# Optimization experiments

Measured on AMD Instinct MI355X. Metric: run time of the kernel, lower is better.

The kernel has to match this reference:

```python
import jax, jax.numpy as jnp
import numpy as np


def setup_inputs() -> dict:
    key = jax.random.key(0)
    k1, k2 = jax.random.split(key)
    T, K, D = 100000, 512, 64
    flags_matrix = jax.random.uniform(k1, (T, K), dtype=jnp.float32)  # ~half > 0.5
    emb_weight = jax.random.normal(k2, (K, D), dtype=jnp.float32)
    return {"flags_matrix": flags_matrix, "emb_weight": emb_weight}


def reference(flags_matrix, emb_weight):
    # mask[t,k] = 1 if flag active; bag-of-embeddings mean over active items per row.
    mask = (flags_matrix > 0.5).astype(emb_weight.dtype)          # [T, K]
    counts = jnp.sum(mask, axis=1, keepdims=True)                  # [T, 1]
    sums = mask @ emb_weight                                       # [T, D] masked sum of embeddings
    # rows with no active flags -> zeros (matches the torch branch)
    return jnp.where(counts > 0, sums / jnp.maximum(counts, 1.0), 0.0)
```

## Files before the change

kernel.cpp:

```cpp
#include <hip/hip_runtime.h>
#include <stdint.h>


#define T_ROWS 100000
#define K_FLAGS 512
#define D_DIM 64
#define TILES (T_ROWS / 16)

typedef __attribute__((ext_vector_type(4))) float f32x4;
typedef __attribute__((ext_vector_type(8))) short bf16x8;

__device__ __forceinline__ uint32_t f32_to_bf16_rne(float f) {
  union { float f; uint32_t u; } v; v.f = f;
  uint32_t u = v.u;
  return (u + 0x7FFFu + ((u >> 16) & 1u)) >> 16;
}

__global__ __launch_bounds__(1024, 8) void flagbag_kernel(const float* __restrict__ flags,
                                                          const float* __restrict__ W,
                                                          float* __restrict__ out) {
  __shared__ uint4 sB[16 * 4 * 64];
  __shared__ uint32_t sM[16][256];

  const int tid = threadIdx.x;

#pragma unroll
  for (int p = 0; p < 4; ++p) {
    const int E  = tid + p * 1024;
    const int s  = E >> 8;
    const int nt = (E >> 6) & 3;
    const int ln = E & 63;
    const int n  = (ln & 15) + 16 * nt;
    const int kq = ln >> 4;
    const int kb = 128 * kq + 8 * s;
    uint32_t r[4];
#pragma unroll
    for (int j = 0; j < 4; ++j) {
      uint32_t lo = f32_to_bf16_rne(W[(size_t)(kb + 2 * j    ) * D_DIM + n]);
      uint32_t hi = f32_to_bf16_rne(W[(size_t)(kb + 2 * j + 1) * D_DIM + n]);
      r[j] = lo | (hi << 16);
    }
    sB[E] = make_uint4(r[0], r[1], r[2], r[3]);
  }
  __syncthreads();

  const int lane = tid & 63;
  const int wave = tid >> 6;
  const int tile = wave * 512 + (int)blockIdx.x;
  if (tile >= TILES) return;

  const int t0 = tile * 16;

  const float* ft = flags + (size_t)t0 * K_FLAGS + lane * 8;

  uint32_t D0 = 0, D1 = 0, D2 = 0, D3 = 0;
  f32x4 ra[4], rb[4];
#pragma unroll
  for (int r = 0; r < 3; ++r) {
    ra[r] = *reinterpret_cast<const f32x4*>(ft + r * K_FLAGS);
    rb[r] = *reinterpret_cast<const f32x4*>(ft + r * K_FLAGS + 4);
  }
#pragma unroll
  for (int r = 0; r < 16; ++r) {
    if (r + 3 < 16) {
      ra[(r + 3) & 3] = *reinterpret_cast<const f32x4*>(ft + (r + 3) * K_FLAGS);
      rb[(r + 3) & 3] = *reinterpret_cast<const f32x4*>(ft + (r + 3) * K_FLAGS + 4);
    }
    const f32x4 a = ra[r & 3], b = rb[r & 3];
    uint32_t byte = 0;
#pragma unroll
    for (int j = 0; j < 4; ++j) {
      byte |= (a[j] > 0.5f) ? (1u << j)       : 0u;
      byte |= (b[j] > 0.5f) ? (1u << (j + 4)) : 0u;
    }
    const uint32_t sh = byte << ((r & 3) * 8);
    if ((r >> 2) == 0) D0 |= sh;
    else if ((r >> 2) == 1) D1 |= sh;
    else if ((r >> 2) == 2) D2 |= sh;
    else D3 |= sh;
  }

  uint32_t* sMw = sM[wave];
  sMw[0 * 64 + (lane ^ 0)]  = D0;
  sMw[1 * 64 + (lane ^ 4)]  = D1;
  sMw[2 * 64 + (lane ^ 8)]  = D2;
  sMw[3 * 64 + (lane ^ 12)] = D3;

  const int m  = lane & 15;
  const int kq = lane >> 4;
  const int mj = m >> 2, mb = m & 3;
  const uint8_t* sMb = reinterpret_cast<const uint8_t*>(sMw);

  uint32_t mbytes[16];
#pragma unroll
  for (int s = 0; s < 16; ++s)
    mbytes[s] = sMb[(size_t)(mj * 64 + ((16 * kq + s) ^ (4 * mj))) * 4 + mb];

  int cnt = 0;
#pragma unroll
  for (int s = 0; s < 16; ++s) cnt += __popc(mbytes[s]);
  cnt += __shfl_xor(cnt, 16);
  cnt += __shfl_xor(cnt, 32);
  const float inv = (cnt > 0) ? (1.0f / (float)cnt) : 0.0f;

  const uint4* sbl = &sB[lane];
  f32x4 acc[4];
#pragma unroll
  for (int nt = 0; nt < 4; ++nt) acc[nt] = (f32x4){0.f, 0.f, 0.f, 0.f};

  uint4 bc[4], bn[4];
#pragma unroll
  for (int nt = 0; nt < 4; ++nt) bc[nt] = sbl[nt * 64];

#pragma unroll
  for (int s = 0; s < 16; ++s) {
    if (s + 1 < 16) {
#pragma unroll
      for (int nt = 0; nt < 4; ++nt) bn[nt] = sbl[((s + 1) * 4 + nt) * 64];
    }
    const uint32_t byte = mbytes[s];
    bf16x8 af;
#pragma unroll
    for (int e = 0; e < 8; ++e) af[e] = ((byte >> e) & 1u) ? (short)0x3F80 : (short)0;

#pragma unroll
    for (int nt = 0; nt < 4; ++nt)
      acc[nt] = __builtin_amdgcn_mfma_f32_16x16x32_bf16(
          af, *reinterpret_cast<const bf16x8*>(&bc[nt]), acc[nt], 0, 0, 0);

#pragma unroll
    for (int nt = 0; nt < 4; ++nt) bc[nt] = bn[nt];
  }

#pragma unroll
  for (int r = 0; r < 4; ++r) {
    const int row = kq * 4 + r;
    const float invr = __shfl(inv, row);
    float* orow = out + (size_t)(t0 + row) * D_DIM + m;
#pragma unroll
    for (int nt = 0; nt < 4; ++nt)
      orow[16 * nt] = acc[nt][r] * invr;
  }
}

extern "C" void kernel_launch(void* const* d_in, const int* in_sizes, int n_in,
                              void* d_out, int out_size, void* d_ws, size_t ws_size,
                              hipStream_t stream) {
  const float* flags = (const float*)d_in[0];
  const float* W     = (const float*)d_in[1];
  float* out         = (float*)d_out;

  hipLaunchKernelGGL(flagbag_kernel, dim3(512), dim3(1024), 0, stream, flags, W, out);
}
```

Measured before the change: 45.69 us.

## Precompute bf16 B fragments in separate kernel and read from global

Moves the per-block conversion of the embedding weights into MFMA bf16 fragments into a small prep kernel that writes a global buffer. The main kernel drops its shared-memory B staging and __syncthreads, reading fragments directly from global/L2, and folds the mask-byte reads and popcount into the MFMA loop. This removes redundant per-block conversion work and the barrier, at the cost of an extra kernel launch and global-memory fragment loads instead of LDS loads inside the inner loop.

```diff
diff --git a/kernel.cpp b/kernel.cpp
--- a/kernel.cpp
+++ b/kernel.cpp
@@ -10,40 +10,37 @@
 typedef __attribute__((ext_vector_type(4))) float f32x4;
 typedef __attribute__((ext_vector_type(8))) short bf16x8;
 
+__device__ uint32_t g_bfrag[16 * 4 * 64 * 4];
+
 __device__ __forceinline__ uint32_t f32_to_bf16_rne(float f) {
   union { float f; uint32_t u; } v; v.f = f;
   uint32_t u = v.u;
   return (u + 0x7FFFu + ((u >> 16) & 1u)) >> 16;
 }
 
+__global__ void prep_b_kernel(const float* __restrict__ W) {
+  int E = blockIdx.x * blockDim.x + threadIdx.x;
+  if (E >= 16 * 4 * 64) return;
+  int lane = E & 63;
+  int nt   = (E >> 6) & 3;
+  int s    = E >> 8;
+  int n    = (lane & 15) + 16 * nt;
+  int kb   = 128 * (lane >> 4) + 8 * s;
+  uint32_t r[4];
+#pragma unroll
+  for (int j = 0; j < 4; ++j) {
+    uint32_t lo = f32_to_bf16_rne(W[(size_t)(kb + 2 * j    ) * D_DIM + n]);
+    uint32_t hi = f32_to_bf16_rne(W[(size_t)(kb + 2 * j + 1) * D_DIM + n]);
+    r[j] = lo | (hi << 16);
+  }
+  *reinterpret_cast<uint4*>(&g_bfrag[(size_t)E * 4]) = make_uint4(r[0], r[1], r[2], r[3]);
+}
+
 __global__ __launch_bounds__(1024, 8) void flagbag_kernel(const float* __restrict__ flags,
-                                                          const float* __restrict__ W,
                                                           float* __restrict__ out) {
-  __shared__ uint4 sB[16 * 4 * 64];
   __shared__ uint32_t sM[16][256];
 
-  const int tid = threadIdx.x;
-
-#pragma unroll
-  for (int p = 0; p < 4; ++p) {
-    const int E  = tid + p * 1024;
-    const int s  = E >> 8;
-    const int nt = (E >> 6) & 3;
-    const int ln = E & 63;
-    const int n  = (ln & 15) + 16 * nt;
-    const int kq = ln >> 4;
-    const int kb = 128 * kq + 8 * s;
-    uint32_t r[4];
-#pragma unroll
-    for (int j = 0; j < 4; ++j) {
-      uint32_t lo = f32_to_bf16_rne(W[(size_t)(kb + 2 * j    ) * D_DIM + n]);
-      uint32_t hi = f32_to_bf16_rne(W[(size_t)(kb + 2 * j + 1) * D_DIM + n]);
-      r[j] = lo | (hi << 16);
-    }
-    sB[E] = make_uint4(r[0], r[1], r[2], r[3]);
-  }
-  __syncthreads();
-
+  const int tid  = threadIdx.x;
   const int lane = tid & 63;
   const int wave = tid >> 6;
   const int tile = wave * 512 + (int)blockIdx.x;
@@ -89,36 +86,29 @@
   const int m  = lane & 15;
   const int kq = lane >> 4;
   const int mj = m >> 2, mb = m & 3;
+  const int m4 = 4 * mj;
   const uint8_t* sMb = reinterpret_cast<const uint8_t*>(sMw);
+  const int C = 4 * (mj * 64 + 16 * kq) + mb;
 
-  uint32_t mbytes[16];
-#pragma unroll
-  for (int s = 0; s < 16; ++s)
-    mbytes[s] = sMb[(size_t)(mj * 64 + ((16 * kq + s) ^ (4 * mj))) * 4 + mb];
+  const uint4* gb = reinterpret_cast<const uint4*>(g_bfrag) + lane;
 
-  int cnt = 0;
-#pragma unroll
-  for (int s = 0; s < 16; ++s) cnt += __popc(mbytes[s]);
-  cnt += __shfl_xor(cnt, 16);
-  cnt += __shfl_xor(cnt, 32);
-  const float inv = (cnt > 0) ? (1.0f / (float)cnt) : 0.0f;
-
-  const uint4* sbl = &sB[lane];
   f32x4 acc[4];
 #pragma unroll
   for (int nt = 0; nt < 4; ++nt) acc[nt] = (f32x4){0.f, 0.f, 0.f, 0.f};
 
   uint4 bc[4], bn[4];
 #pragma unroll
-  for (int nt = 0; nt < 4; ++nt) bc[nt] = sbl[nt * 64];
+  for (int nt = 0; nt < 4; ++nt) bc[nt] = gb[nt * 64];
 
+  int cnt = 0;
 #pragma unroll
   for (int s = 0; s < 16; ++s) {
     if (s + 1 < 16) {
 #pragma unroll
-      for (int nt = 0; nt < 4; ++nt) bn[nt] = sbl[((s + 1) * 4 + nt) * 64];
+      for (int nt = 0; nt < 4; ++nt) bn[nt] = gb[((s + 1) * 4 + nt) * 64];
     }
-    const uint32_t byte = mbytes[s];
+    const uint32_t byte = sMb[C + 4 * (s ^ m4)];
+    cnt += __popc(byte);
     bf16x8 af;
 #pragma unroll
     for (int e = 0; e < 8; ++e) af[e] = ((byte >> e) & 1u) ? (short)0x3F80 : (short)0;
@@ -131,6 +121,10 @@
 #pragma unroll
     for (int nt = 0; nt < 4; ++nt) bc[nt] = bn[nt];
   }
+
+  cnt += __shfl_xor(cnt, 16);
+  cnt += __shfl_xor(cnt, 32);
+  const float inv = (cnt > 0) ? (1.0f / (float)cnt) : 0.0f;
 
 #pragma unroll
   for (int r = 0; r < 4; ++r) {
@@ -150,5 +144,6 @@
   const float* W     = (const float*)d_in[1];
   float* out         = (float*)d_out;
 
-  hipLaunchKernelGGL(flagbag_kernel, dim3(512), dim3(1024), 0, stream, flags, W, out);
+  hipLaunchKernelGGL(prep_b_kernel, dim3(16), dim3(256), 0, stream, W);
+  hipLaunchKernelGGL(flagbag_kernel, dim3(512), dim3(1024), 0, stream, flags, out);
 }
```

After: 51.08 us. +11.8%, slower.
